# Optimization experiments

Measured on AMD Instinct MI355X. Metric: run time of the kernel, lower is better.

## Reference

```python
import jax, jax.numpy as jnp
import numpy as np

NUM_USER = 100000
NUM_ENT = 100000
NUM_REL = 60
NUM_ITEM = 20000
ITEM_NUM_IN_KG = 20000
DIM = 64
N_NEIGHBOR = 8
N_ITER = 2
BATCH = 16384


def setup_inputs() -> dict:
    key = jax.random.key(0)
    ks = jax.random.split(key, 10)
    return {
        "u": jax.random.randint(ks[0], (BATCH,), 0, NUM_USER),
        "v": jax.random.randint(ks[1], (BATCH,), 0, NUM_ITEM),
        "usr_emb": jax.random.normal(ks[2], (NUM_USER, DIM), jnp.float32),
        "item_emb": jax.random.normal(ks[3], (NUM_ITEM, DIM), jnp.float32),
        "ent_emb": jax.random.normal(ks[4], (NUM_ENT + 1, DIM), jnp.float32),
        "rel_emb": jax.random.normal(ks[5], (NUM_REL + 1, DIM), jnp.float32),
        "W": jax.random.normal(ks[6], (DIM, DIM), jnp.float32) / np.sqrt(DIM),
        "b": jax.random.normal(ks[7], (DIM,), jnp.float32) * 0.01,
        "adj_ent": jax.random.randint(ks[8], (NUM_ENT + 1, N_NEIGHBOR), 0, NUM_ENT + 1),
        "adj_rel": jax.random.randint(ks[9], (NUM_ENT + 1, N_NEIGHBOR), 0, NUM_REL + 1),
    }


def reference(u, v, usr_emb, item_emb, ent_emb, rel_emb, W, b, adj_ent, adj_rel):
    B = u.shape[0]
    ue = usr_emb[u]  # [B, D]

    # hop-0 indices: items not in the KG map to the padding entity for neighbor lookup
    v_clip = jnp.where(v >= ITEM_NUM_IN_KG, NUM_ENT, v)
    ents = [v_clip[:, None]]  # [B, 1]
    rels = []
    for h in range(N_ITER):
        rels.append(adj_rel[ents[h]].reshape(B, -1))  # [B, 8**(h+1)]
        ents.append(adj_ent[ents[h]].reshape(B, -1))

    # hop-0 embedding uses the ORIGINAL v via the item table (entities[0][:] = v)
    ev = [item_emb[v[:, None]]] + [ent_emb[e] for e in ents[1:]]  # each [B, m, D]
    rv = [rel_emb[r] for r in rels]

    for i in range(N_ITER):
        act = jnp.tanh if i == N_ITER - 1 else jax.nn.sigmoid
        nxt = []
        for hop in range(N_ITER - i):
            sv = ev[hop]  # [B, m, D]
            m = sv.shape[1]
            nv = ev[hop + 1].reshape(B, m, N_NEIGHBOR, DIM)
            nr = rv[hop].reshape(B, m, N_NEIGHBOR, DIM)
            # user-relation attention over the 8 sampled neighbors
            scores = jnp.einsum("bd,bmnd->bmn", ue, nr)
            wgt = jax.nn.softmax(scores, axis=-1)
            agg = jnp.einsum("bmn,bmnd->bmd", wgt, nv)
            out = (sv + agg) @ W.T + b  # 'sum' aggregator
            nxt.append(act(out))
        ev = nxt

    item_vec = ev[0].reshape(B, DIM)
    return jax.nn.sigmoid(jnp.sum(ue * item_vec, axis=1))  # [B]
```

## Files before the change

kernel.cpp:

```cpp
#include <hip/hip_runtime.h>


namespace {

constexpr int kDim      = 64;
constexpr int kNN       = 8;
constexpr int kNumEnt   = 100000;
constexpr int kItemInKG = 20000;
constexpr int kElems    = 8;
constexpr int kVecs     = 9;
constexpr int kRelChunks = 976;

__device__ __forceinline__ float fast_sigmoid(float x) {
  return 1.0f / (1.0f + __expf(-x));
}
__device__ __forceinline__ float fast_tanh(float x) {
  return 2.0f / (1.0f + __expf(-2.0f * x)) - 1.0f;
}
__device__ __forceinline__ float readlane_f(float v, int lane) {
  return __int_as_float(__builtin_amdgcn_readlane(__float_as_int(v), lane));
}

__global__ void __launch_bounds__(kElems * 64)
kgcn_kernel(const int* __restrict__ u, const int* __restrict__ v,
            const float* __restrict__ usr_emb, const float* __restrict__ item_emb,
            const float* __restrict__ ent_emb, const float* __restrict__ rel_emb,
            const float* __restrict__ W, const float* __restrict__ bias,
            const int* __restrict__ adj_ent, const int* __restrict__ adj_rel,
            float* __restrict__ out)
{
  const int tid = threadIdx.x;
  const int wv  = tid >> 6;
  const int ln  = tid & 63;
  const int b   = blockIdx.x * kElems + wv;

  __shared__ float4 s_w4[kDim * 16];
  __shared__ float  s_relt[kDim * 65];
  __shared__ __align__(16) float s_pre[kElems][kVecs][kDim];

  const float4* W4 = reinterpret_cast<const float4*>(W);
  const float4* R4 = reinterpret_cast<const float4*>(rel_emb);
  const float4 wst0 = W4[tid];
  const float4 wst1 = W4[512 + tid];
  const float4 rst0 = R4[tid];
  const float4 rst1 = (512 + tid < kRelChunks) ? R4[512 + tid]
                                               : make_float4(0.f, 0.f, 0.f, 0.f);

  const int   uid = u[b];
  const int   vid = v[b];
  const float ue  = usr_emb[(size_t)uid * kDim + ln];
  const float ev0 = item_emb[(size_t)vid * kDim + ln];
  const int   e0  = (vid >= kItemInKG) ? kNumEnt : vid;

  int e1v = 0, r1v = 0;
  if (ln < kNN) {
    e1v = adj_ent[(size_t)e0 * kNN + ln];
    r1v = adj_rel[(size_t)e0 * kNN + ln];
  }
  const int parent = __shfl(e1v, ln >> 3, 64);
  const int e2v    = adj_ent[(size_t)parent * kNN + (ln & 7)];
  const int r2v    = adj_rel[(size_t)parent * kNN + (ln & 7)];

  {
    int id = tid, row = id >> 4, col = id & 15;
    s_w4[(row << 4) | (col & 8) | ((col ^ row) & 7)] = wst0;
    id = 512 + tid; row = id >> 4; col = id & 15;
    s_w4[(row << 4) | (col & 8) | ((col ^ row) & 7)] = wst1;
  }
  {
    int id = tid, r = id >> 4, c = (id & 15) << 2;
    s_relt[(c + 0) * 65 + r] = rst0.x;
    s_relt[(c + 1) * 65 + r] = rst0.y;
    s_relt[(c + 2) * 65 + r] = rst0.z;
    s_relt[(c + 3) * 65 + r] = rst0.w;
    id = 512 + tid; r = id >> 4; c = (id & 15) << 2;
    s_relt[(c + 0) * 65 + r] = rst1.x;
    s_relt[(c + 1) * 65 + r] = rst1.y;
    s_relt[(c + 2) * 65 + r] = rst1.z;
    s_relt[(c + 3) * 65 + r] = rst1.w;
  }

  float ev1r[kNN];
  #pragma unroll
  for (int m = 0; m < kNN; ++m)
    ev1r[m] = ent_emb[(size_t)__builtin_amdgcn_readlane(e1v, m) * kDim + ln];

  __syncthreads();

  float t;
  {
    const float* relc = &s_relt[ln];
    float a0 = 0.f, a1 = 0.f, a2 = 0.f, a3 = 0.f;
    #pragma unroll
    for (int k = 0; k < kDim; k += 4) {
      a0 = fmaf(readlane_f(ue, k + 0), relc[(k + 0) * 65], a0);
      a1 = fmaf(readlane_f(ue, k + 1), relc[(k + 1) * 65], a1);
      a2 = fmaf(readlane_f(ue, k + 2), relc[(k + 2) * 65], a2);
      a3 = fmaf(readlane_f(ue, k + 3), relc[(k + 3) * 65], a3);
    }
    t = (a0 + a1) + (a2 + a3);
  }

  float w2v;
  {
    const float s2 = __shfl(t, r2v, 64);
    float mx = s2;
    #pragma unroll
    for (int m = 1; m <= 4; m <<= 1) mx = fmaxf(mx, __shfl_xor(mx, m, 64));
    const float e = __expf(s2 - mx);
    float sm = e;
    #pragma unroll
    for (int m = 1; m <= 4; m <<= 1) sm += __shfl_xor(sm, m, 64);
    w2v = e / sm;
  }
  float w0v;
  {
    const float s0 = __shfl(t, r1v, 64);
    float mx = s0;
    #pragma unroll
    for (int m = 1; m <= 4; m <<= 1) mx = fmaxf(mx, __shfl_xor(mx, m, 64));
    w0v = __expf(s0 - mx);
    float sm = w0v;
    #pragma unroll
    for (int m = 1; m <= 4; m <<= 1) sm += __shfl_xor(sm, m, 64);
    w0v /= sm;
  }

  {
    float agg = 0.f;
    #pragma unroll
    for (int n = 0; n < kNN; ++n)
      agg = fmaf(readlane_f(w0v, n), ev1r[n], agg);
    s_pre[wv][0][ln] = ev0 + agg;
  }
  #pragma unroll 2
  for (int m = 0; m < kNN; ++m) {
    float acc = 0.f;
    #pragma unroll
    for (int n = 0; n < kNN; ++n) {
      const int e2u = __builtin_amdgcn_readlane(e2v, m * kNN + n);
      acc = fmaf(readlane_f(w2v, m * kNN + n),
                 ent_emb[(size_t)e2u * kDim + ln], acc);
    }
    s_pre[wv][1 + m][ln] = ev1r[m] + acc;
  }

  float4 Wreg[16];
  #pragma unroll
  for (int k4 = 0; k4 < 16; ++k4)
    Wreg[k4] = s_w4[(ln << 4) | (k4 & 8) | ((k4 ^ ln) & 7)];

  const float bln = bias[ln];

  float h[kVecs];
  #pragma unroll
  for (int m = 0; m < kVecs; ++m) {
    const float* p0 = &s_pre[wv][m][0];
    float acc = 0.f;
    #pragma unroll
    for (int q = 0; q < 16; ++q) {
      const float4 p = *reinterpret_cast<const float4*>(p0 + (q << 2));
      acc = fmaf(Wreg[q].x, p.x, acc);
      acc = fmaf(Wreg[q].y, p.y, acc);
      acc = fmaf(Wreg[q].z, p.z, acc);
      acc = fmaf(Wreg[q].w, p.w, acc);
    }
    h[m] = fast_sigmoid(acc + bln);
  }

  {
    float pre = h[0];
    #pragma unroll
    for (int n = 0; n < kNN; ++n)
      pre = fmaf(readlane_f(w0v, n), h[1 + n], pre);
    s_pre[wv][0][ln] = pre;
  }

  {
    const float* p0 = &s_pre[wv][0][0];
    float acc = 0.f;
    #pragma unroll
    for (int q = 0; q < 16; ++q) {
      const float4 p = *reinterpret_cast<const float4*>(p0 + (q << 2));
      acc = fmaf(Wreg[q].x, p.x, acc);
      acc = fmaf(Wreg[q].y, p.y, acc);
      acc = fmaf(Wreg[q].z, p.z, acc);
      acc = fmaf(Wreg[q].w, p.w, acc);
    }
    const float item = fast_tanh(acc + bln);
    float tt = ue * item;
    #pragma unroll
    for (int off = 32; off > 0; off >>= 1)
      tt += __shfl_xor(tt, off, 64);
    if (ln == 0) out[b] = fast_sigmoid(tt);
  }
}

}

extern "C" void kernel_launch(void* const* d_in, const int* in_sizes, int n_in,
                              void* d_out, int out_size, void* d_ws, size_t ws_size,
                              hipStream_t stream) {
  const int*   u        = (const int*)d_in[0];
  const int*   v        = (const int*)d_in[1];
  const float* usr_emb  = (const float*)d_in[2];
  const float* item_emb = (const float*)d_in[3];
  const float* ent_emb  = (const float*)d_in[4];
  const float* rel_emb  = (const float*)d_in[5];
  const float* W        = (const float*)d_in[6];
  const float* bias     = (const float*)d_in[7];
  const int*   adj_ent  = (const int*)d_in[8];
  const int*   adj_rel  = (const int*)d_in[9];
  float*       out      = (float*)d_out;

  const int B = in_sizes[0];
  dim3 grid(B / kElems), block(kElems * 64);
  hipLaunchKernelGGL(kgcn_kernel, grid, block, 0, stream,
                     u, v, usr_emb, item_emb, ent_emb, rel_emb, W, bias,
                     adj_ent, adj_rel, out);
}
```

Baseline: 64.79 us.

## Convert entity table to fp16 in workspace and use packed FMA for W matvec

Adds a pre-pass kernel that converts the whole entity embedding table to fp16 in the workspace on every call, so the main kernel's random neighbor gathers read half the bytes. It also rewrites the W matrix-vector products to use v_pk_fma_f32 on float pairs. The conversion pass reads the full 25.6 MB table and writes 12.8 MB each call, which likely costs more than the gather traffic it saves, since only about 1.2M rows of the table are touched. fp16 storage also lowers the precision of entity embeddings.

New measurement: 66.30 us. 1.02x slower.

```diff
diff --git a/kernel.cpp b/kernel.cpp
--- a/kernel.cpp
+++ b/kernel.cpp
@@ -1,4 +1,5 @@
 #include <hip/hip_runtime.h>
+#include <hip/hip_fp16.h>
 
 
 namespace {
@@ -10,6 +11,9 @@
 constexpr int kElems    = 8;
 constexpr int kVecs     = 9;
 constexpr int kRelChunks = 976;
+constexpr size_t kEntHalfBytes = (size_t)(kNumEnt + 1) * kDim * sizeof(__half);
+
+typedef float v2f __attribute__((ext_vector_type(2)));
 
 __device__ __forceinline__ float fast_sigmoid(float x) {
   return 1.0f / (1.0f + __expf(-x));
@@ -20,11 +24,26 @@
 __device__ __forceinline__ float readlane_f(float v, int lane) {
   return __int_as_float(__builtin_amdgcn_readlane(__float_as_int(v), lane));
 }
-
+__device__ __forceinline__ void pk_fma(v2f& acc, v2f a, v2f b) {
+  asm("v_pk_fma_f32 %0, %1, %2, %0" : "+v"(acc) : "v"(a), "v"(b));
+}
+
+__global__ void __launch_bounds__(256)
+conv_kernel(const float* __restrict__ src, __half2* __restrict__ dst, int n4) {
+  const int i = blockIdx.x * 256 + threadIdx.x;
+  if (i < n4) {
+    const float4 f = reinterpret_cast<const float4*>(src)[i];
+    dst[2 * i + 0] = __floats2half2_rn(f.x, f.y);
+    dst[2 * i + 1] = __floats2half2_rn(f.z, f.w);
+  }
+}
+
+template <bool HALF>
 __global__ void __launch_bounds__(kElems * 64)
 kgcn_kernel(const int* __restrict__ u, const int* __restrict__ v,
             const float* __restrict__ usr_emb, const float* __restrict__ item_emb,
-            const float* __restrict__ ent_emb, const float* __restrict__ rel_emb,
+            const float* __restrict__ ent_emb, const __half* __restrict__ ent_h,
+            const float* __restrict__ rel_emb,
             const float* __restrict__ W, const float* __restrict__ bias,
             const int* __restrict__ adj_ent, const int* __restrict__ adj_rel,
             float* __restrict__ out)
@@ -82,8 +101,10 @@
 
   float ev1r[kNN];
   #pragma unroll
-  for (int m = 0; m < kNN; ++m)
-    ev1r[m] = ent_emb[(size_t)__builtin_amdgcn_readlane(e1v, m) * kDim + ln];
+  for (int m = 0; m < kNN; ++m) {
+    const size_t row = (size_t)__builtin_amdgcn_readlane(e1v, m) * kDim + ln;
+    ev1r[m] = HALF ? __half2float(ent_h[row]) : ent_emb[row];
+  }
 
   __syncthreads();
 
@@ -138,17 +159,21 @@
     float acc = 0.f;
     #pragma unroll
     for (int n = 0; n < kNN; ++n) {
-      const int e2u = __builtin_amdgcn_readlane(e2v, m * kNN + n);
-      acc = fmaf(readlane_f(w2v, m * kNN + n),
-                 ent_emb[(size_t)e2u * kDim + ln], acc);
+      const size_t row =
+          (size_t)__builtin_amdgcn_readlane(e2v, m * kNN + n) * kDim + ln;
+      const float g = HALF ? __half2float(ent_h[row]) : ent_emb[row];
+      acc = fmaf(readlane_f(w2v, m * kNN + n), g, acc);
     }
     s_pre[wv][1 + m][ln] = ev1r[m] + acc;
   }
 
-  float4 Wreg[16];
+  v2f Wp[32];
   #pragma unroll
-  for (int k4 = 0; k4 < 16; ++k4)
-    Wreg[k4] = s_w4[(ln << 4) | (k4 & 8) | ((k4 ^ ln) & 7)];
+  for (int k4 = 0; k4 < 16; ++k4) {
+    const float4 wq = s_w4[(ln << 4) | (k4 & 8) | ((k4 ^ ln) & 7)];
+    Wp[2 * k4 + 0] = v2f{wq.x, wq.y};
+    Wp[2 * k4 + 1] = v2f{wq.z, wq.w};
+  }
 
   const float bln = bias[ln];
 
@@ -156,16 +181,14 @@
   #pragma unroll
   for (int m = 0; m < kVecs; ++m) {
     const float* p0 = &s_pre[wv][m][0];
-    float acc = 0.f;
+    v2f acc01 = v2f{0.f, 0.f}, acc23 = v2f{0.f, 0.f};
     #pragma unroll
     for (int q = 0; q < 16; ++q) {
       const float4 p = *reinterpret_cast<const float4*>(p0 + (q << 2));
-      acc = fmaf(Wreg[q].x, p.x, acc);
-      acc = fmaf(Wreg[q].y, p.y, acc);
-      acc = fmaf(Wreg[q].z, p.z, acc);
-      acc = fmaf(Wreg[q].w, p.w, acc);
-    }
-    h[m] = fast_sigmoid(acc + bln);
+      pk_fma(acc01, Wp[2 * q + 0], v2f{p.x, p.y});
+      pk_fma(acc23, Wp[2 * q + 1], v2f{p.z, p.w});
+    }
+    h[m] = fast_sigmoid((acc01.x + acc01.y) + (acc23.x + acc23.y) + bln);
   }
 
   {
@@ -178,16 +201,15 @@
 
   {
     const float* p0 = &s_pre[wv][0][0];
-    float acc = 0.f;
+    v2f acc01 = v2f{0.f, 0.f}, acc23 = v2f{0.f, 0.f};
     #pragma unroll
     for (int q = 0; q < 16; ++q) {
       const float4 p = *reinterpret_cast<const float4*>(p0 + (q << 2));
-      acc = fmaf(Wreg[q].x, p.x, acc);
-      acc = fmaf(Wreg[q].y, p.y, acc);
-      acc = fmaf(Wreg[q].z, p.z, acc);
-      acc = fmaf(Wreg[q].w, p.w, acc);
-    }
-    const float item = fast_tanh(acc + bln);
+      pk_fma(acc01, Wp[2 * q + 0], v2f{p.x, p.y});
+      pk_fma(acc23, Wp[2 * q + 1], v2f{p.z, p.w});
+    }
+    const float item =
+        fast_tanh((acc01.x + acc01.y) + (acc23.x + acc23.y) + bln);
     float tt = ue * item;
     #pragma unroll
     for (int off = 32; off > 0; off >>= 1)
@@ -215,7 +237,19 @@
 
   const int B = in_sizes[0];
   dim3 grid(B / kElems), block(kElems * 64);
-  hipLaunchKernelGGL(kgcn_kernel, grid, block, 0, stream,
-                     u, v, usr_emb, item_emb, ent_emb, rel_emb, W, bias,
-                     adj_ent, adj_rel, out);
-}
+
+  const bool use_half = (ws_size >= kEntHalfBytes);
+  if (use_half) {
+    __half* ent_h = (__half*)d_ws;
+    const int n4 = (kNumEnt + 1) * kDim / 4;
+    hipLaunchKernelGGL(conv_kernel, dim3((n4 + 255) / 256), dim3(256), 0,
+                       stream, ent_emb, (__half2*)ent_h, n4);
+    hipLaunchKernelGGL((kgcn_kernel<true>), grid, block, 0, stream,
+                       u, v, usr_emb, item_emb, ent_emb, ent_h, rel_emb, W,
+                       bias, adj_ent, adj_rel, out);
+  } else {
+    hipLaunchKernelGGL((kgcn_kernel<false>), grid, block, 0, stream,
+                       u, v, usr_emb, item_emb, ent_emb, (const __half*)d_ws,
+                       rel_emb, W, bias, adj_ent, adj_rel, out);
+  }
+}
```
